# Performance work log

Measured on AMD Instinct MI355X. Metric: run time of the kernel, lower is better.

## Reference

```python
import jax, jax.numpy as jnp
import numpy as np

T, B = 4096, 32
EP_LEN = 256
K = T // EP_LEN          # episodes per trajectory
LM = EP_LEN              # max episode length
S_DIM, C_DIM, M_DIM, L_DIM = 128, 32, 32, 32
E_S, E_C, H, A = 128, 64, 256, 16


def setup_inputs() -> dict:
    key = jax.random.key(0)
    ks = jax.random.split(key, 16)
    f = lambda i, shape: jax.random.normal(ks[i], shape, jnp.float32)
    inp = {
        "state": f(0, (T, B, S_DIM)),
        "latent_mean": f(1, (T, B, L_DIM)) * 0.1,
        "latent_logvar": f(2, (T, B, L_DIM)) * 0.1,
        "latent_mean_t": f(3, (T, B, L_DIM)) * 0.1,
        "latent_logvar_t": f(4, (T, B, L_DIM)) * 0.1,
        "agent_character": f(5, (T, B, C_DIM)),
        "mental_state": f(6, (T, B, M_DIM)),
        "partner_actions": jax.random.randint(ks[7], (LM, B), 0, A, jnp.int32),
    }
    # episode boundaries: done at the last step of each EP_LEN-long episode
    t = jnp.arange(T)
    inp["dones"] = jnp.broadcast_to(((t + 1) % EP_LEN == 0).astype(jnp.float32)[:, None], (T, B))
    sc = lambda fan: 1.0 / np.sqrt(fan)
    inp["W_se"] = f(8, (S_DIM, E_S)) * sc(S_DIM); inp["b_se"] = jnp.zeros((E_S,), jnp.float32)
    inp["W_ce"] = f(9, (C_DIM, E_C)) * sc(C_DIM); inp["b_ce"] = jnp.zeros((E_C,), jnp.float32)
    inp["W_sa"] = f(10, (E_S + E_C, H)) * sc(E_S + E_C); inp["b_sa"] = jnp.zeros((H,), jnp.float32)
    inp["W_h"] = f(11, (E_C + M_DIM, H)) * sc(E_C + M_DIM); inp["b_h"] = jnp.zeros((H,), jnp.float32)
    inp["Wi"] = f(12, (H, 3 * H)) * sc(H); inp["bi"] = jnp.zeros((3 * H,), jnp.float32)
    inp["Wh"] = f(13, (H, 3 * H)) * sc(H); inp["bh"] = jnp.zeros((3 * H,), jnp.float32)
    inp["W_out"] = f(14, (H, A)) * sc(H); inp["b_out"] = jnp.zeros((A,), jnp.float32)
    return inp


def _gru(h, x, Wi, bi, Wh, bh):
    gi = x @ Wi + bi
    gh = h @ Wh + bh
    ir, iz, inn = jnp.split(gi, 3, axis=-1)
    hr, hz, hn = jnp.split(gh, 3, axis=-1)
    r = jax.nn.sigmoid(ir + hr)
    z = jax.nn.sigmoid(iz + hz)
    n = jnp.tanh(inn + r * hn)
    return (1.0 - z) * n + z * h


def _episode_layout(d):  # d: [T] float dones -> (episode_id, pos_in_episode)
    started = jnp.concatenate([jnp.zeros((1,), bool), d[:-1] > 0.5])
    ep = jnp.cumsum(started.astype(jnp.int32))
    t = jnp.arange(d.shape[0])
    start = jax.lax.cummax(jnp.where(started, t, 0))
    return ep, t - start


def _to_episodes(x, ep, pos):  # x: [T, F] -> [K, LM, F]  (transform_timestep_to_batch)
    return jnp.zeros((K, LM) + x.shape[1:], x.dtype).at[ep, pos].set(x, mode="drop")


def _shift_padding_to_front(out, mask):  # out: [K, LM, D], mask: [K, LM]
    cnt = mask.sum(-1).astype(jnp.int32)
    src = jnp.arange(LM)[None, :] - (LM - cnt)[:, None]
    idx = jnp.clip(src, 0, LM - 1)
    ok = (src >= 0).astype(out.dtype)
    shifted = jnp.take_along_axis(out, idx[:, :, None], axis=1) * ok[:, :, None]
    return shifted, jnp.take_along_axis(mask, idx, axis=1) * ok


def _forward(state, latent_mean, latent_logvar, latent_mean_t, latent_logvar_t,
             agent_character, mental_state, partner_actions, dones,
             W_se, b_se, W_ce, b_ce, W_sa, b_sa, W_h, b_h, Wi, bi, Wh, bh, W_out, b_out):
    # ---- KL between consecutive-timestep posteriors ----
    lm = jnp.concatenate((latent_mean, latent_mean_t), axis=-1)
    lv = jnp.concatenate((latent_logvar, latent_logvar_t), axis=-1)
    gauss_dim = lm.shape[-1]
    all_m = jnp.concatenate((jnp.zeros((1,) + lm.shape[1:], lm.dtype), lm), axis=0)
    all_lv = jnp.concatenate((jnp.zeros((1,) + lv.shape[1:], lv.dtype), lv), axis=0)
    mu, m = all_m[1:], all_m[:-1]
    logE, logS = all_lv[1:], all_lv[:-1]
    kl = 0.5 * (jnp.sum(logS, -1) - jnp.sum(logE, -1) - gauss_dim
                + jnp.sum(jnp.exp(logE - logS), -1)
                + jnp.sum((m - mu) * (m - mu) / jnp.exp(logS), -1))  # [T,B]
    kl_loss = kl.sum(0).sum(0).mean()

    # ---- embeddings ----
    se = jax.nn.relu(state @ W_se + b_se)                         # [T,B,E_S]
    ce = jax.nn.relu(agent_character @ W_ce + b_ce)               # [T,B,E_C]
    sa = jnp.concatenate((se, ce), -1) @ W_sa + b_sa              # [T,B,H]
    hid = jnp.concatenate((ce, mental_state), -1) @ W_h + b_h     # [T,B,H]

    # ---- split trajectories into episodes (gather/scatter) ----
    ep, pos = jax.vmap(_episode_layout, in_axes=1, out_axes=0)(dones)  # [B,T] each
    to_ep = jax.vmap(_to_episodes, in_axes=(1, 0, 0), out_axes=0)
    k_sa = to_ep(sa, ep, pos)                                     # [B,K,LM,H]
    k_hid = to_ep(hid, ep, pos)                                   # [B,K,LM,H]
    k_d = to_ep(dones[..., None], ep, pos)[..., 0]                # [B,K,LM]
    mask = jax.vmap(lambda e, p: jnp.zeros((K, LM), jnp.float32).at[e, p].set(1.0, mode="drop"))(ep, pos)

    # ---- sequential RNN scan per episode (vectorized over B*K) ----
    h0 = k_hid[:, :, 0, :]                                        # [B,K,H]
    xs = (jnp.moveaxis(k_sa, 2, 0), jnp.moveaxis(k_hid, 2, 0), jnp.moveaxis(k_d, 2, 0))

    def step(h, xt):
        sa_t, hid_t, d_t = xt
        h = jnp.where(d_t[..., None] > 0.5, hid_t, h)             # reset to per-step init on done
        h = _gru(h, sa_t, Wi, bi, Wh, bh)
        return h, h

    _, ys = jax.lax.scan(step, h0, xs)                            # [LM,B,K,H]
    ys = jnp.moveaxis(ys, 0, 2)                                   # [B,K,LM,H]

    logits = (ys @ W_out + b_out) * mask[..., None]               # [B,K,LM,A]
    shifted, _ = jax.vmap(_shift_padding_to_front)(logits, mask)
    out = jnp.moveaxis(shifted.sum(1), 0, 1)                      # [LM,B,A]

    logp = jnp.take_along_axis(jax.nn.log_softmax(out, -1), partner_actions[..., None], -1)[..., 0]
    return kl_loss, logp.sum(-1)                                  # scalar, [LM]


def reference(state, latent_mean, latent_logvar, latent_mean_t, latent_logvar_t,
              agent_character, mental_state, partner_actions, dones,
              W_se, b_se, W_ce, b_ce, W_sa, b_sa, W_h, b_h, Wi, bi, Wh, bh, W_out, b_out):
    return _forward(state, latent_mean, latent_logvar, latent_mean_t, latent_logvar_t,
                    agent_character, mental_state, partner_actions, dones,
                    W_se, b_se, W_ce, b_ce, W_sa, b_sa, W_h, b_h, Wi, bi, Wh, bh, W_out, b_out)
```

## Files before the change

### kernel.cpp

```cpp
#include <hip/hip_runtime.h>
#include <math.h>

typedef short bf16x8 __attribute__((ext_vector_type(8)));
typedef float f32x4 __attribute__((ext_vector_type(4)));
typedef unsigned short u16;
typedef unsigned int u32;

#define T_DIM 4096
#define B_DIM 32

static constexpr size_t OFF_SE     = 0;
static constexpr size_t OFF_CE     = 33554432;
static constexpr size_t OFF_SA     = 50331648;
static constexpr size_t OFF_HID    = 117440512;
static constexpr size_t OFF_WHT    = 117964800;
static constexpr size_t OFF_WIT    = 118358016;
static constexpr size_t OFF_OUTACC = 118751232;
static constexpr size_t OFF_KLP    = 119799808;

__device__ __forceinline__ u16 f2bf(float x) {
    u32 b = __float_as_uint(x);
    u32 lsb = (b >> 16) & 1u;
    b += 0x7fffu + lsb;
    return (u16)(b >> 16);
}
__device__ __forceinline__ float bf2f(u16 u) {
    return __uint_as_float(((u32)u) << 16);
}
__device__ __forceinline__ float fsig(float x) {
    x = fminf(fmaxf(x, -30.f), 30.f);
    float e = __expf(x);
    return __fdividef(e, e + 1.f);
}
__device__ __forceinline__ float ftanh(float x) {
    x = fminf(fmaxf(x, -15.f), 15.f);
    float e = __expf(2.f * x);
    return __fdividef(e - 1.f, e + 1.f);
}

__global__ __launch_bounds__(256) void prep_kernel(const float* __restrict__ Wh,
                                                   const float* __restrict__ Wi,
                                                   u16* __restrict__ WhT,
                                                   u16* __restrict__ WiT) {
    int idx = blockIdx.x * 256 + threadIdx.x;
    if (idx < 196608) {
        int n = idx >> 8, k = idx & 255;
        WhT[idx] = f2bf(Wh[k * 768 + n]);
    } else {
        int i = idx - 196608;
        int n = i >> 8, k = i & 255;
        WiT[i] = f2bf(Wi[k * 768 + n]);
    }
}

#define KLTERM(MU, LE, M, LS)                   \
    do {                                        \
        float _ls = (LS), _le = (LE);           \
        sS += _ls; sE += _le;                   \
        float _es = expf(-_ls);                 \
        sX += expf(_le) * _es;                  \
        float _dm = (M) - (MU);                 \
        sQ += _dm * _dm * _es;                  \
    } while (0)

__global__ __launch_bounds__(256) void kl_kernel(const float* __restrict__ lm,
                                                 const float* __restrict__ lv,
                                                 const float* __restrict__ lmt,
                                                 const float* __restrict__ lvt,
                                                 float* __restrict__ klp) {
    __shared__ float red[256];
    int tid = threadIdx.x;
    int idx = blockIdx.x * 256 + tid;
    float sS = 0.f, sE = 0.f, sX = 0.f, sQ = 0.f;
    const int cur = idx * 32;
    const int prv = cur - B_DIM * 32;
    const bool hasprev = (idx >= B_DIM);
    for (int half = 0; half < 2; half++) {
        const float* pm = half ? lmt : lm;
        const float* pv = half ? lvt : lv;
        for (int ch = 0; ch < 8; ch++) {
            float4 mu = *(const float4*)&pm[cur + ch * 4];
            float4 le = *(const float4*)&pv[cur + ch * 4];
            float4 m = make_float4(0.f, 0.f, 0.f, 0.f);
            float4 ls = make_float4(0.f, 0.f, 0.f, 0.f);
            if (hasprev) {
                m = *(const float4*)&pm[prv + ch * 4];
                ls = *(const float4*)&pv[prv + ch * 4];
            }
            KLTERM(mu.x, le.x, m.x, ls.x);
            KLTERM(mu.y, le.y, m.y, ls.y);
            KLTERM(mu.z, le.z, m.z, ls.z);
            KLTERM(mu.w, le.w, m.w, ls.w);
        }
    }
    float kl = 0.5f * (sS - sE - 64.0f + sX + sQ);
    red[tid] = kl;
    __syncthreads();
    for (int s = 128; s > 0; s >>= 1) {
        if (tid < s) red[tid] += red[tid + s];
        __syncthreads();
    }
    if (tid == 0) klp[blockIdx.x] = red[0];
}

__global__ __launch_bounds__(256) void gemm_k(const float* __restrict__ A32a,
                                              const u16* __restrict__ A16a,
                                              const u16* __restrict__ A16b,
                                              const float* __restrict__ W,
                                              const float* __restrict__ bias,
                                              u16* __restrict__ out,
                                              int mode, int K, int N, int do_relu) {
    __shared__ __align__(16) u16 As[64 * 40];
    __shared__ __align__(16) u16 Bs[64 * 40];
    const int tid = threadIdx.x;
    const int rows0 = blockIdx.x * 64;
    const int cols0 = blockIdx.y * 64;
    const int w16 = tid >> 6;
    const int lane = tid & 63;
    const int quad = lane >> 4;
    const int l15 = lane & 15;
    f32x4 acc[4];
    for (int i = 0; i < 4; i++) acc[i] = (f32x4){0.f, 0.f, 0.f, 0.f};
    const int nsteps = K >> 5;
    const int arow = tid >> 2, aseg = (tid & 3) << 3;
    const int bk = tid >> 3, bseg = (tid & 7) << 3;
    for (int ks = 0; ks < nsteps; ks++) {
        const int grow = rows0 + arow;
        const int k0 = ks * 32 + aseg;
        if (mode == 0) {
            float4 v0 = *(const float4*)&A32a[grow * 128 + k0];
            float4 v1 = *(const float4*)&A32a[grow * 128 + k0 + 4];
            u16* d = &As[arow * 40 + aseg];
            d[0] = f2bf(v0.x); d[1] = f2bf(v0.y); d[2] = f2bf(v0.z); d[3] = f2bf(v0.w);
            d[4] = f2bf(v1.x); d[5] = f2bf(v1.y); d[6] = f2bf(v1.z); d[7] = f2bf(v1.w);
        } else if (mode == 1) {
            float4 v0 = *(const float4*)&A32a[grow * 32 + k0];
            float4 v1 = *(const float4*)&A32a[grow * 32 + k0 + 4];
            u16* d = &As[arow * 40 + aseg];
            d[0] = f2bf(v0.x); d[1] = f2bf(v0.y); d[2] = f2bf(v0.z); d[3] = f2bf(v0.w);
            d[4] = f2bf(v1.x); d[5] = f2bf(v1.y); d[6] = f2bf(v1.z); d[7] = f2bf(v1.w);
        } else if (mode == 2) {
            bf16x8 v = (k0 < 128) ? *(const bf16x8*)&A16a[grow * 128 + k0]
                                  : *(const bf16x8*)&A16b[grow * 64 + (k0 - 128)];
            *(bf16x8*)&As[arow * 40 + aseg] = v;
        } else {
            const int k6 = grow >> 6, w = (grow >> 5) & 1, bb = grow & 31;
            const int trow = (k6 * 256 + w * 255) * B_DIM + bb;
            for (int j = 0; j < 8; j++) {
                const int k = k0 + j;
                float v = (k < 64) ? bf2f(A16a[trow * 64 + k]) : A32a[trow * 32 + (k - 64)];
                As[arow * 40 + aseg + j] = f2bf(v);
            }
        }
        const int gk = ks * 32 + bk;
        {
            float4 w0 = *(const float4*)&W[gk * N + cols0 + bseg];
            float4 w1 = *(const float4*)&W[gk * N + cols0 + bseg + 4];
            Bs[(bseg + 0) * 40 + bk] = f2bf(w0.x);
            Bs[(bseg + 1) * 40 + bk] = f2bf(w0.y);
            Bs[(bseg + 2) * 40 + bk] = f2bf(w0.z);
            Bs[(bseg + 3) * 40 + bk] = f2bf(w0.w);
            Bs[(bseg + 4) * 40 + bk] = f2bf(w1.x);
            Bs[(bseg + 5) * 40 + bk] = f2bf(w1.y);
            Bs[(bseg + 6) * 40 + bk] = f2bf(w1.z);
            Bs[(bseg + 7) * 40 + bk] = f2bf(w1.w);
        }
        __syncthreads();
        bf16x8 af = *(const bf16x8*)&As[(w16 * 16 + l15) * 40 + quad * 8];
        for (int nt = 0; nt < 4; nt++) {
            bf16x8 bfr = *(const bf16x8*)&Bs[(nt * 16 + l15) * 40 + quad * 8];
            acc[nt] = __builtin_amdgcn_mfma_f32_16x16x32_bf16(af, bfr, acc[nt], 0, 0, 0);
        }
        __syncthreads();
    }
    for (int nt = 0; nt < 4; nt++) {
        const int c = cols0 + nt * 16 + l15;
        const float bv = bias[c];
        for (int r = 0; r < 4; r++) {
            const int row = rows0 + w16 * 16 + quad * 4 + r;
            float v = acc[nt][r] + bv;
            if (do_relu) v = fmaxf(v, 0.f);
            out[row * N + c] = f2bf(v);
        }
    }
}

__global__ void __launch_bounds__(512)
__attribute__((amdgpu_waves_per_eu(2, 2)))
gru6_kernel(const u16* __restrict__ hid,
            const u16* __restrict__ sa,
            const u16* __restrict__ WhT,
            const u16* __restrict__ WiT,
            const float* __restrict__ Wout,
            const float* __restrict__ bi,
            const float* __restrict__ bh,
            u16* __restrict__ gic_all,
            float* __restrict__ outacc) {
    __shared__ __align__(16) u16 whL[8 * 16 * 264];
    __shared__ __align__(16) u16 stage[64 * 264];
    __shared__ __align__(16) u16 hB[16 * 264];
    __shared__ __align__(16) u16 WoL[16 * 264];
    __shared__ float bfold[768];
    __shared__ float bhnL[256];
    const int blk = blockIdx.x;
    const int b = blk >> 1, half = blk & 1;
    const int tid = threadIdx.x;
    const int lane = tid & 63, wv = tid >> 6;
    const int quad = lane >> 4, l15 = lane & 15;
    const int c0 = (tid & 63) * 4;
    u16* gic = gic_all + (size_t)blk * (256 * 768);

    for (int i = tid; i < 4096; i += 512) {
        const int s = i >> 9, rr = (i >> 5) & 15, seg = (i & 31) * 8;
        const int g = s * 6 + 5;
        *(bf16x8*)&whL[(s * 16 + rr) * 264 + seg] = *(const bf16x8*)&WhT[(g * 16 + rr) * 256 + seg];
    }
    for (int i = tid; i < 4096; i += 512) {
        const int a = i >> 8, k = i & 255;
        WoL[a * 264 + k] = f2bf(Wout[k * 16 + a]);
    }
    for (int c = tid; c < 768; c += 512) bfold[c] = (c < 512) ? (bi[c] + bh[c]) : bi[c];
    if (tid < 256) bhnL[tid] = bh[512 + tid];
    float hreg[4];
    {
        ushort4 hv = *(const ushort4*)&hid[(size_t)((((half << 3) + wv) << 6) + b) * 256 + c0];
        hreg[0] = bf2f(hv.x); hreg[1] = bf2f(hv.y);
        hreg[2] = bf2f(hv.z); hreg[3] = bf2f(hv.w);
        *(ushort4*)&hB[wv * 264 + c0] = hv;
        ushort4 z = make_ushort4(0, 0, 0, 0);
        *(ushort4*)&hB[(8 + wv) * 264 + c0] = z;
    }
    __syncthreads();

    bf16x8 wreg[5][8];
    for (int ch = 0; ch < 8; ch++) {
        for (int as = 0; as < 4; as++) {
            __syncthreads();
#pragma unroll
            for (int j = 0; j < 4; j++) {
                const int lin = j * 512 + tid;
                const int row = lin >> 5, seg = (lin & 31) * 8;
                const int pcs = as * 8 + (row >> 3), sql = row & 7;
                const int t = ((half << 3) + sql) * 256 + ch * 32 + pcs;
                *(bf16x8*)&stage[row * 264 + seg] =
                    *(const bf16x8*)&sa[((size_t)(t * 32 + b)) * 256 + seg];
            }
            __syncthreads();
            bf16x8 afr[4][8];
#pragma unroll
            for (int mt = 0; mt < 4; mt++)
#pragma unroll
                for (int ks = 0; ks < 8; ks++)
                    afr[mt][ks] = *(const bf16x8*)&stage[(mt * 16 + l15) * 264 + ks * 32 + quad * 8];
            bf16x8 wc[8], wn[8];
            {
                const u16* p = &WiT[((wv * 6) * 16 + l15) * 256 + quad * 8];
#pragma unroll
                for (int ks = 0; ks < 8; ks++) wc[ks] = *(const bf16x8*)&p[ks * 32];
            }
            for (int j = 0; j < 6; j++) {
                if (j < 5) {
                    const u16* p = &WiT[((wv * 6 + j + 1) * 16 + l15) * 256 + quad * 8];
#pragma unroll
                    for (int ks = 0; ks < 8; ks++) wn[ks] = *(const bf16x8*)&p[ks * 32];
                }
                const float bf = bfold[(wv * 6 + j) * 16 + l15];
#pragma unroll
                for (int mt = 0; mt < 4; mt++) {
                    f32x4 acc = (f32x4){0.f, 0.f, 0.f, 0.f};
#pragma unroll
                    for (int ks = 0; ks < 8; ks++)
                        acc = __builtin_amdgcn_mfma_f32_16x16x32_bf16(afr[mt][ks], wc[ks], acc, 0, 0, 0);
                    const int rbase = as * 64 + mt * 16 + quad * 4;
#pragma unroll
                    for (int r = 0; r < 4; r++)
                        gic[(size_t)(rbase + r) * 768 + (wv * 6 + j) * 16 + l15] = f2bf(acc[r] + bf);
                }
#pragma unroll
                for (int ks = 0; ks < 8; ks++) wc[ks] = wn[ks];
            }
        }
#pragma unroll
        for (int j = 0; j < 5; j++) {
            const u16* p = &WhT[((wv * 6 + j) * 16 + l15) * 256 + quad * 8];
#pragma unroll
            for (int ks = 0; ks < 8; ks++) wreg[j][ks] = *(const bf16x8*)&p[ks * 32];
        }
        for (int pc = 0; pc < 32; pc++) {
            const int POS = ch * 32 + pc;
            __syncthreads();
            const u16* gp = &gic[(size_t)(pc * 8 + wv) * 768];
            ushort4 g_r = *(const ushort4*)&gp[c0];
            ushort4 g_z = *(const ushort4*)&gp[256 + c0];
            ushort4 g_n = *(const ushort4*)&gp[512 + c0];
            bf16x8 af[8];
            if (POS == 255) {
                const u16* hp = &hid[(size_t)((((half << 3) + (l15 & 7)) << 6) + 32 + b) * 256 + quad * 8];
#pragma unroll
                for (int ks = 0; ks < 8; ks++) af[ks] = *(const bf16x8*)&hp[ks * 32];
            } else {
#pragma unroll
                for (int ks = 0; ks < 8; ks++)
                    af[ks] = *(const bf16x8*)&hB[l15 * 264 + ks * 32 + quad * 8];
            }
            if (wv == 7 && POS > 0) {
                f32x4 acc = (f32x4){0.f, 0.f, 0.f, 0.f};
#pragma unroll
                for (int ks = 0; ks < 8; ks++) {
                    bf16x8 al = *(const bf16x8*)&hB[l15 * 264 + ks * 32 + quad * 8];
                    bf16x8 wo = *(const bf16x8*)&WoL[l15 * 264 + ks * 32 + quad * 8];
                    acc = __builtin_amdgcn_mfma_f32_16x16x32_bf16(al, wo, acc, 0, 0, 0);
                }
                float s = acc[0] + acc[1] + acc[2] + acc[3];
                s += __shfl_down(s, 32);
                s += __shfl_down(s, 16);
                if (lane < 16)
                    outacc[(size_t)half * 131072 + ((size_t)(POS - 1) * B_DIM + b) * 16 + lane] = s;
            }
#pragma unroll
            for (int j = 0; j < 5; j++) {
                f32x4 acc = (f32x4){0.f, 0.f, 0.f, 0.f};
#pragma unroll
                for (int ks = 0; ks < 8; ks++)
                    acc = __builtin_amdgcn_mfma_f32_16x16x32_bf16(af[ks], wreg[j][ks], acc, 0, 0, 0);
                const int t = wv * 6 + j;
#pragma unroll
                for (int r = 0; r < 4; r++)
                    stage[(quad * 4 + r) * 776 + t * 16 + l15] = f2bf(acc[r]);
            }
            {
                const u16* p = &whL[(wv * 16 + l15) * 264 + quad * 8];
                f32x4 acc = (f32x4){0.f, 0.f, 0.f, 0.f};
#pragma unroll
                for (int ks = 0; ks < 8; ks++)
                    acc = __builtin_amdgcn_mfma_f32_16x16x32_bf16(af[ks], *(const bf16x8*)&p[ks * 32], acc, 0, 0, 0);
                const int t = wv * 6 + 5;
#pragma unroll
                for (int r = 0; r < 4; r++)
                    stage[(quad * 4 + r) * 776 + t * 16 + l15] = f2bf(acc[r]);
            }
            __syncthreads();
            if (POS == 255) {
                ushort4 hv = *(const ushort4*)&hid[(size_t)((((half << 3) + wv) << 6) + 32 + b) * 256 + c0];
                hreg[0] = bf2f(hv.x); hreg[1] = bf2f(hv.y);
                hreg[2] = bf2f(hv.z); hreg[3] = bf2f(hv.w);
            }
            ushort4 h_r = *(const ushort4*)&stage[wv * 776 + c0];
            ushort4 h_z = *(const ushort4*)&stage[wv * 776 + 256 + c0];
            ushort4 h_n = *(const ushort4*)&stage[wv * 776 + 512 + c0];
            const u16* grp = (const u16*)&g_r; const u16* gzp = (const u16*)&g_z;
            const u16* gnp = (const u16*)&g_n;
            const u16* hrp = (const u16*)&h_r; const u16* hzp = (const u16*)&h_z;
            const u16* hnp = (const u16*)&h_n;
            ushort4 hp4;
            u16* ho = (u16*)&hp4;
#pragma unroll
            for (int j = 0; j < 4; j++) {
                const float rv = fsig(bf2f(grp[j]) + bf2f(hrp[j]));
                const float zv = fsig(bf2f(gzp[j]) + bf2f(hzp[j]));
                const float nv = ftanh(bf2f(gnp[j]) + rv * (bf2f(hnp[j]) + bhnL[c0 + j]));
                hreg[j] = (1.f - zv) * nv + zv * hreg[j];
                ho[j] = f2bf(hreg[j]);
            }
            *(ushort4*)&hB[wv * 264 + c0] = hp4;
        }
    }
    __syncthreads();
    if (wv == 7) {
        f32x4 acc = (f32x4){0.f, 0.f, 0.f, 0.f};
#pragma unroll
        for (int ks = 0; ks < 8; ks++) {
            bf16x8 al = *(const bf16x8*)&hB[l15 * 264 + ks * 32 + quad * 8];
            bf16x8 wo = *(const bf16x8*)&WoL[l15 * 264 + ks * 32 + quad * 8];
            acc = __builtin_amdgcn_mfma_f32_16x16x32_bf16(al, wo, acc, 0, 0, 0);
        }
        float s = acc[0] + acc[1] + acc[2] + acc[3];
        s += __shfl_down(s, 32);
        s += __shfl_down(s, 16);
        if (lane < 16)
            outacc[(size_t)half * 131072 + ((size_t)255 * B_DIM + b) * 16 + lane] = s;
    }
}

__global__ __launch_bounds__(64) void final_kernel(const float* __restrict__ outacc,
                                                   const int* __restrict__ pa,
                                                   const float* __restrict__ klp,
                                                   const float* __restrict__ bout,
                                                   float* __restrict__ dout) {
    const int lane = threadIdx.x;
    if (blockIdx.x == 256) {
        float s = 0.f;
        for (int j = 0; j < 8; j++) s += klp[lane + 64 * j];
        for (int off = 32; off > 0; off >>= 1) s += __shfl_down(s, off);
        if (lane == 0) dout[0] = s;
        return;
    }
    const int pos = blockIdx.x;
    float lp = 0.f;
    if (lane < 32) {
        const float* r0 = outacc + ((size_t)pos * B_DIM + lane) * 16;
        const float* r1 = r0 + 131072;
        float v[16];
        float mx = -1e30f;
#pragma unroll
        for (int a = 0; a < 16; a++) {
            v[a] = r0[a] + r1[a] + 16.0f * bout[a];
            mx = fmaxf(mx, v[a]);
        }
        float s = 0.f;
#pragma unroll
        for (int a = 0; a < 16; a++) s += expf(v[a] - mx);
        const int ai = pa[pos * B_DIM + lane];
        lp = v[ai] - mx - logf(s);
    }
    for (int off = 16; off > 0; off >>= 1) lp += __shfl_down(lp, off);
    if (lane == 0) dout[1 + pos] = lp;
}

extern "C" void kernel_launch(void* const* d_in, const int* in_sizes, int n_in,
                              void* d_out, int out_size, void* d_ws, size_t ws_size,
                              hipStream_t stream) {
    const float* state = (const float*)d_in[0];
    const float* lm    = (const float*)d_in[1];
    const float* lv    = (const float*)d_in[2];
    const float* lmt   = (const float*)d_in[3];
    const float* lvt   = (const float*)d_in[4];
    const float* ach   = (const float*)d_in[5];
    const float* ms    = (const float*)d_in[6];
    const int*   pa    = (const int*)d_in[7];
    const float* W_se  = (const float*)d_in[9];
    const float* b_se  = (const float*)d_in[10];
    const float* W_ce  = (const float*)d_in[11];
    const float* b_ce  = (const float*)d_in[12];
    const float* W_sa  = (const float*)d_in[13];
    const float* b_sa  = (const float*)d_in[14];
    const float* W_h   = (const float*)d_in[15];
    const float* b_h   = (const float*)d_in[16];
    const float* Wi    = (const float*)d_in[17];
    const float* bi    = (const float*)d_in[18];
    const float* Wh    = (const float*)d_in[19];
    const float* bh    = (const float*)d_in[20];
    const float* Wout  = (const float*)d_in[21];
    const float* bout  = (const float*)d_in[22];

    char* ws = (char*)d_ws;
    u16* se   = (u16*)(ws + OFF_SE);
    u16* ce   = (u16*)(ws + OFF_CE);
    u16* sa   = (u16*)(ws + OFF_SA);
    u16* hid  = (u16*)(ws + OFF_HID);
    u16* WhT  = (u16*)(ws + OFF_WHT);
    u16* WiT  = (u16*)(ws + OFF_WIT);
    float* outacc = (float*)(ws + OFF_OUTACC);
    float* klp    = (float*)(ws + OFF_KLP);
    float* dout   = (float*)d_out;

    prep_kernel<<<1536, 256, 0, stream>>>(Wh, Wi, WhT, WiT);
    kl_kernel<<<512, 256, 0, stream>>>(lm, lv, lmt, lvt, klp);
    gemm_k<<<dim3(2048, 2), 256, 0, stream>>>(state, nullptr, nullptr, W_se, b_se, se, 0, 128, 128, 1);
    gemm_k<<<dim3(2048, 1), 256, 0, stream>>>(ach, nullptr, nullptr, W_ce, b_ce, ce, 1, 32, 64, 1);
    gemm_k<<<dim3(2048, 4), 256, 0, stream>>>(nullptr, se, ce, W_sa, b_sa, sa, 2, 192, 256, 0);
    gemm_k<<<dim3(16, 4), 256, 0, stream>>>(ms, ce, nullptr, W_h, b_h, hid, 5, 96, 256, 0);
    gru6_kernel<<<64, 512, 0, stream>>>(hid, sa, WhT, WiT, Wout, bi, bh, se, outacc);
    final_kernel<<<257, 64, 0, stream>>>(outacc, pa, klp, bout, dout);
}
```

Baseline: 1.669 ms.

## Keep GRU gate accumulators in registers with double-buffered hidden state

Each wave now computes the r, z and n gate tiles for its own hidden columns, so the recurrent MFMA results stay in registers instead of round-tripping through LDS. This removes one of the two barriers per timestep, and the hidden state is double-buffered in LDS. LDS tiles get an XOR swizzle to cut bank conflicts, and the gic layout is interleaved so each lane fetches its r/z/n inputs in one load. The per-step output projection moves out of the recurrence: summed hidden states go to global memory and the final kernel multiplies them by W_out. The trade-off is more global writes and a heavier final kernel, and only half the lanes do the gate math.

```diff
diff --git a/kernel.cpp b/kernel.cpp
--- a/kernel.cpp
+++ b/kernel.cpp
@@ -187,48 +187,58 @@
 
 __global__ void __launch_bounds__(512)
 __attribute__((amdgpu_waves_per_eu(2, 2)))
-gru6_kernel(const u16* __restrict__ hid,
+gru8_kernel(const u16* __restrict__ hid,
             const u16* __restrict__ sa,
             const u16* __restrict__ WhT,
             const u16* __restrict__ WiT,
-            const float* __restrict__ Wout,
             const float* __restrict__ bi,
             const float* __restrict__ bh,
             u16* __restrict__ gic_all,
-            float* __restrict__ outacc) {
+            float* __restrict__ hsum) {
     __shared__ __align__(16) u16 whL[8 * 16 * 264];
     __shared__ __align__(16) u16 stage[64 * 264];
-    __shared__ __align__(16) u16 hB[16 * 264];
-    __shared__ __align__(16) u16 WoL[16 * 264];
+    __shared__ __align__(16) u16 hB[2][16 * 264];
     __shared__ float bfold[768];
-    __shared__ float bhnL[256];
     const int blk = blockIdx.x;
     const int b = blk >> 1, half = blk & 1;
     const int tid = threadIdx.x;
     const int lane = tid & 63, wv = tid >> 6;
     const int quad = lane >> 4, l15 = lane & 15;
-    const int c0 = (tid & 63) * 4;
-    u16* gic = gic_all + (size_t)blk * (256 * 768);
+    const int c0j0 = wv * 32 + l15;
+    u16* gic = gic_all + (size_t)blk * (256 * 1024);
+    const int gts[6] = {2 * wv, 2 * wv + 1, 16 + 2 * wv, 17 + 2 * wv, 32 + 2 * wv, 33 + 2 * wv};
 
     for (int i = tid; i < 4096; i += 512) {
         const int s = i >> 9, rr = (i >> 5) & 15, seg = (i & 31) * 8;
-        const int g = s * 6 + 5;
-        *(bf16x8*)&whL[(s * 16 + rr) * 264 + seg] = *(const bf16x8*)&WhT[(g * 16 + rr) * 256 + seg];
-    }
-    for (int i = tid; i < 4096; i += 512) {
-        const int a = i >> 8, k = i & 255;
-        WoL[a * 264 + k] = f2bf(Wout[k * 16 + a]);
+        const int g = 33 + 2 * s;
+        *(bf16x8*)&whL[(s * 16 + rr) * 264 + (seg ^ ((rr & 7) << 3))] =
+            *(const bf16x8*)&WhT[(g * 16 + rr) * 256 + seg];
     }
     for (int c = tid; c < 768; c += 512) bfold[c] = (c < 512) ? (bi[c] + bh[c]) : bi[c];
-    if (tid < 256) bhnL[tid] = bh[512 + tid];
-    float hreg[4];
-    {
-        ushort4 hv = *(const ushort4*)&hid[(size_t)((((half << 3) + wv) << 6) + b) * 256 + c0];
-        hreg[0] = bf2f(hv.x); hreg[1] = bf2f(hv.y);
-        hreg[2] = bf2f(hv.z); hreg[3] = bf2f(hv.w);
-        *(ushort4*)&hB[wv * 264 + c0] = hv;
-        ushort4 z = make_ushort4(0, 0, 0, 0);
-        *(ushort4*)&hB[(8 + wv) * 264 + c0] = z;
+    const float bhn0 = bh[512 + c0j0];
+    const float bhn1 = bh[512 + c0j0 + 16];
+    float hreg[2][4] = {{0.f, 0.f, 0.f, 0.f}, {0.f, 0.f, 0.f, 0.f}};
+    if (quad < 2) {
+#pragma unroll
+        for (int j = 0; j < 2; j++)
+#pragma unroll
+            for (int r = 0; r < 4; r++) {
+                const int rw = quad * 4 + r;
+                const int c = c0j0 + 16 * j;
+                u16 hv = hid[(size_t)((((half << 3) + rw) << 6) + b) * 256 + c];
+                hreg[j][r] = bf2f(hv);
+                hB[0][rw * 264 + (c ^ ((rw & 7) << 3))] = hv;
+            }
+    } else {
+#pragma unroll
+        for (int j = 0; j < 2; j++)
+#pragma unroll
+            for (int r = 0; r < 4; r++) {
+                const int rw = quad * 4 + r;
+                const int c = c0j0 + 16 * j;
+                hB[0][rw * 264 + (c ^ ((rw & 7) << 3))] = 0;
+                hB[1][rw * 264 + (c ^ ((rw & 7) << 3))] = 0;
+            }
     }
     __syncthreads();
 
@@ -242,7 +252,7 @@
                 const int row = lin >> 5, seg = (lin & 31) * 8;
                 const int pcs = as * 8 + (row >> 3), sql = row & 7;
                 const int t = ((half << 3) + sql) * 256 + ch * 32 + pcs;
-                *(bf16x8*)&stage[row * 264 + seg] =
+                *(bf16x8*)&stage[row * 264 + (seg ^ ((row & 7) << 3))] =
                     *(const bf16x8*)&sa[((size_t)(t * 32 + b)) * 256 + seg];
             }
             __syncthreads();
@@ -251,20 +261,23 @@
             for (int mt = 0; mt < 4; mt++)
 #pragma unroll
                 for (int ks = 0; ks < 8; ks++)
-                    afr[mt][ks] = *(const bf16x8*)&stage[(mt * 16 + l15) * 264 + ks * 32 + quad * 8];
+                    afr[mt][ks] = *(const bf16x8*)&stage[(mt * 16 + l15) * 264 +
+                                                         ((ks * 32 + quad * 8) ^ ((l15 & 7) << 3))];
             bf16x8 wc[8], wn[8];
             {
-                const u16* p = &WiT[((wv * 6) * 16 + l15) * 256 + quad * 8];
+                const u16* p = &WiT[(size_t)(gts[0] * 16 + l15) * 256 + quad * 8];
 #pragma unroll
                 for (int ks = 0; ks < 8; ks++) wc[ks] = *(const bf16x8*)&p[ks * 32];
             }
-            for (int j = 0; j < 6; j++) {
-                if (j < 5) {
-                    const u16* p = &WiT[((wv * 6 + j + 1) * 16 + l15) * 256 + quad * 8];
+#pragma unroll
+            for (int jj = 0; jj < 6; jj++) {
+                if (jj < 5) {
+                    const u16* p = &WiT[(size_t)(gts[jj + 1] * 16 + l15) * 256 + quad * 8];
 #pragma unroll
                     for (int ks = 0; ks < 8; ks++) wn[ks] = *(const bf16x8*)&p[ks * 32];
                 }
-                const float bf = bfold[(wv * 6 + j) * 16 + l15];
+                const float bf = bfold[gts[jj] * 16 + l15];
+                const int cp = ((2 * wv + (jj & 1)) * 16 + l15) * 4 + (jj >> 1);
 #pragma unroll
                 for (int mt = 0; mt < 4; mt++) {
                     f32x4 acc = (f32x4){0.f, 0.f, 0.f, 0.f};
@@ -274,7 +287,7 @@
                     const int rbase = as * 64 + mt * 16 + quad * 4;
 #pragma unroll
                     for (int r = 0; r < 4; r++)
-                        gic[(size_t)(rbase + r) * 768 + (wv * 6 + j) * 16 + l15] = f2bf(acc[r] + bf);
+                        gic[(size_t)(rbase + r) * 1024 + cp] = f2bf(acc[r] + bf);
                 }
 #pragma unroll
                 for (int ks = 0; ks < 8; ks++) wc[ks] = wn[ks];
@@ -282,17 +295,26 @@
         }
 #pragma unroll
         for (int j = 0; j < 5; j++) {
-            const u16* p = &WhT[((wv * 6 + j) * 16 + l15) * 256 + quad * 8];
+            const u16* p = &WhT[(size_t)(gts[j] * 16 + l15) * 256 + quad * 8];
 #pragma unroll
             for (int ks = 0; ks < 8; ks++) wreg[j][ks] = *(const bf16x8*)&p[ks * 32];
         }
+        __syncthreads();
         for (int pc = 0; pc < 32; pc++) {
             const int POS = ch * 32 + pc;
-            __syncthreads();
-            const u16* gp = &gic[(size_t)(pc * 8 + wv) * 768];
-            ushort4 g_r = *(const ushort4*)&gp[c0];
-            ushort4 g_z = *(const ushort4*)&gp[256 + c0];
-            ushort4 g_n = *(const ushort4*)&gp[512 + c0];
+            const u16* hr = hB[POS & 1];
+            u16* hw = hB[(POS + 1) & 1];
+            ushort4 gi4[2][4];
+            if (quad < 2) {
+#pragma unroll
+                for (int j = 0; j < 2; j++)
+#pragma unroll
+                    for (int r = 0; r < 4; r++) {
+                        const int rw = quad * 4 + r;
+                        gi4[j][r] = *(const ushort4*)&gic[(size_t)(pc * 8 + rw) * 1024 +
+                                                          (size_t)(c0j0 + 16 * j) * 4];
+                    }
+            }
             bf16x8 af[8];
             if (POS == 255) {
                 const u16* hp = &hid[(size_t)((((half << 3) + (l15 & 7)) << 6) + 32 + b) * 256 + quad * 8];
@@ -301,90 +323,67 @@
             } else {
 #pragma unroll
                 for (int ks = 0; ks < 8; ks++)
-                    af[ks] = *(const bf16x8*)&hB[l15 * 264 + ks * 32 + quad * 8];
-            }
-            if (wv == 7 && POS > 0) {
-                f32x4 acc = (f32x4){0.f, 0.f, 0.f, 0.f};
+                    af[ks] = *(const bf16x8*)&hr[l15 * 264 + ((ks * 32 + quad * 8) ^ ((l15 & 7) << 3))];
+            }
+            f32x4 acc[6];
+#pragma unroll
+            for (int jj = 0; jj < 6; jj++) acc[jj] = (f32x4){0.f, 0.f, 0.f, 0.f};
+#pragma unroll
+            for (int jj = 0; jj < 5; jj++)
+#pragma unroll
+                for (int ks = 0; ks < 8; ks++)
+                    acc[jj] = __builtin_amdgcn_mfma_f32_16x16x32_bf16(af[ks], wreg[jj][ks], acc[jj], 0, 0, 0);
+            {
+                const u16* p = &whL[(wv * 16 + l15) * 264];
 #pragma unroll
                 for (int ks = 0; ks < 8; ks++) {
-                    bf16x8 al = *(const bf16x8*)&hB[l15 * 264 + ks * 32 + quad * 8];
-                    bf16x8 wo = *(const bf16x8*)&WoL[l15 * 264 + ks * 32 + quad * 8];
-                    acc = __builtin_amdgcn_mfma_f32_16x16x32_bf16(al, wo, acc, 0, 0, 0);
+                    bf16x8 wf = *(const bf16x8*)&p[(ks * 32 + quad * 8) ^ ((l15 & 7) << 3)];
+                    acc[5] = __builtin_amdgcn_mfma_f32_16x16x32_bf16(af[ks], wf, acc[5], 0, 0, 0);
                 }
-                float s = acc[0] + acc[1] + acc[2] + acc[3];
-                s += __shfl_down(s, 32);
-                s += __shfl_down(s, 16);
-                if (lane < 16)
-                    outacc[(size_t)half * 131072 + ((size_t)(POS - 1) * B_DIM + b) * 16 + lane] = s;
-            }
-#pragma unroll
-            for (int j = 0; j < 5; j++) {
-                f32x4 acc = (f32x4){0.f, 0.f, 0.f, 0.f};
-#pragma unroll
-                for (int ks = 0; ks < 8; ks++)
-                    acc = __builtin_amdgcn_mfma_f32_16x16x32_bf16(af[ks], wreg[j][ks], acc, 0, 0, 0);
-                const int t = wv * 6 + j;
-#pragma unroll
-                for (int r = 0; r < 4; r++)
-                    stage[(quad * 4 + r) * 776 + t * 16 + l15] = f2bf(acc[r]);
-            }
-            {
-                const u16* p = &whL[(wv * 16 + l15) * 264 + quad * 8];
-                f32x4 acc = (f32x4){0.f, 0.f, 0.f, 0.f};
-#pragma unroll
-                for (int ks = 0; ks < 8; ks++)
-                    acc = __builtin_amdgcn_mfma_f32_16x16x32_bf16(af[ks], *(const bf16x8*)&p[ks * 32], acc, 0, 0, 0);
-                const int t = wv * 6 + 5;
-#pragma unroll
-                for (int r = 0; r < 4; r++)
-                    stage[(quad * 4 + r) * 776 + t * 16 + l15] = f2bf(acc[r]);
+            }
+            if (POS == 255 && quad < 2) {
+#pragma unroll
+                for (int j = 0; j < 2; j++)
+#pragma unroll
+                    for (int r = 0; r < 4; r++) {
+                        const int rw = quad * 4 + r;
+                        hreg[j][r] = bf2f(hid[(size_t)((((half << 3) + rw) << 6) + 32 + b) * 256 +
+                                              (c0j0 + 16 * j)]);
+                    }
+            }
+            float l4[2] = {0.f, 0.f};
+            if (quad < 2) {
+#pragma unroll
+                for (int j = 0; j < 2; j++) {
+                    const float bhn = j ? bhn1 : bhn0;
+#pragma unroll
+                    for (int r = 0; r < 4; r++) {
+                        const int rw = quad * 4 + r;
+                        const float rv = fsig(bf2f(gi4[j][r].x) + acc[j][r]);
+                        const float zv = fsig(bf2f(gi4[j][r].y) + acc[2 + j][r]);
+                        const float nv = ftanh(bf2f(gi4[j][r].z) + rv * (acc[4 + j][r] + bhn));
+                        hreg[j][r] = (1.f - zv) * nv + zv * hreg[j][r];
+                        l4[j] += hreg[j][r];
+                        hw[rw * 264 + ((c0j0 + 16 * j) ^ ((rw & 7) << 3))] = f2bf(hreg[j][r]);
+                    }
+                }
+            }
+            float t0 = l4[0] + __shfl_down(l4[0], 16);
+            float t1 = l4[1] + __shfl_down(l4[1], 16);
+            if (quad == 0) {
+                float* hp = hsum + (size_t)half * 2097152 + ((size_t)POS * 32 + b) * 256 + c0j0;
+                hp[0] = t0;
+                hp[16] = t1;
             }
             __syncthreads();
-            if (POS == 255) {
-                ushort4 hv = *(const ushort4*)&hid[(size_t)((((half << 3) + wv) << 6) + 32 + b) * 256 + c0];
-                hreg[0] = bf2f(hv.x); hreg[1] = bf2f(hv.y);
-                hreg[2] = bf2f(hv.z); hreg[3] = bf2f(hv.w);
-            }
-            ushort4 h_r = *(const ushort4*)&stage[wv * 776 + c0];
-            ushort4 h_z = *(const ushort4*)&stage[wv * 776 + 256 + c0];
-            ushort4 h_n = *(const ushort4*)&stage[wv * 776 + 512 + c0];
-            const u16* grp = (const u16*)&g_r; const u16* gzp = (const u16*)&g_z;
-            const u16* gnp = (const u16*)&g_n;
-            const u16* hrp = (const u16*)&h_r; const u16* hzp = (const u16*)&h_z;
-            const u16* hnp = (const u16*)&h_n;
-            ushort4 hp4;
-            u16* ho = (u16*)&hp4;
-#pragma unroll
-            for (int j = 0; j < 4; j++) {
-                const float rv = fsig(bf2f(grp[j]) + bf2f(hrp[j]));
-                const float zv = fsig(bf2f(gzp[j]) + bf2f(hzp[j]));
-                const float nv = ftanh(bf2f(gnp[j]) + rv * (bf2f(hnp[j]) + bhnL[c0 + j]));
-                hreg[j] = (1.f - zv) * nv + zv * hreg[j];
-                ho[j] = f2bf(hreg[j]);
-            }
-            *(ushort4*)&hB[wv * 264 + c0] = hp4;
-        }
-    }
-    __syncthreads();
-    if (wv == 7) {
-        f32x4 acc = (f32x4){0.f, 0.f, 0.f, 0.f};
-#pragma unroll
-        for (int ks = 0; ks < 8; ks++) {
-            bf16x8 al = *(const bf16x8*)&hB[l15 * 264 + ks * 32 + quad * 8];
-            bf16x8 wo = *(const bf16x8*)&WoL[l15 * 264 + ks * 32 + quad * 8];
-            acc = __builtin_amdgcn_mfma_f32_16x16x32_bf16(al, wo, acc, 0, 0, 0);
-        }
-        float s = acc[0] + acc[1] + acc[2] + acc[3];
-        s += __shfl_down(s, 32);
-        s += __shfl_down(s, 16);
-        if (lane < 16)
-            outacc[(size_t)half * 131072 + ((size_t)255 * B_DIM + b) * 16 + lane] = s;
-    }
-}
-
-__global__ __launch_bounds__(64) void final_kernel(const float* __restrict__ outacc,
+        }
+    }
+}
+
+__global__ __launch_bounds__(64) void final_kernel(const float* __restrict__ hsum,
                                                    const int* __restrict__ pa,
                                                    const float* __restrict__ klp,
+                                                   const float* __restrict__ Wout,
                                                    const float* __restrict__ bout,
                                                    float* __restrict__ dout) {
     const int lane = threadIdx.x;
@@ -395,18 +394,33 @@
         if (lane == 0) dout[0] = s;
         return;
     }
+    __shared__ float WoS[4096];
+    for (int i = lane; i < 4096; i += 64) WoS[i] = Wout[i];
+    __syncthreads();
     const int pos = blockIdx.x;
     float lp = 0.f;
     if (lane < 32) {
-        const float* r0 = outacc + ((size_t)pos * B_DIM + lane) * 16;
-        const float* r1 = r0 + 131072;
+        const float* h0 = hsum + ((size_t)pos * B_DIM + lane) * 256;
+        const float* h1 = h0 + 2097152;
         float v[16];
+#pragma unroll
+        for (int a = 0; a < 16; a++) v[a] = 16.0f * bout[a];
+        for (int k4 = 0; k4 < 64; k4++) {
+            float4 a0 = *(const float4*)&h0[k4 * 4];
+            float4 a1 = *(const float4*)&h1[k4 * 4];
+            const float hk0 = a0.x + a1.x, hk1 = a0.y + a1.y;
+            const float hk2 = a0.z + a1.z, hk3 = a0.w + a1.w;
+            const float* w0 = &WoS[(k4 * 4 + 0) * 16];
+            const float* w1 = &WoS[(k4 * 4 + 1) * 16];
+            const float* w2 = &WoS[(k4 * 4 + 2) * 16];
+            const float* w3 = &WoS[(k4 * 4 + 3) * 16];
+#pragma unroll
+            for (int a = 0; a < 16; a++)
+                v[a] += hk0 * w0[a] + hk1 * w1[a] + hk2 * w2[a] + hk3 * w3[a];
+        }
         float mx = -1e30f;
 #pragma unroll
-        for (int a = 0; a < 16; a++) {
-            v[a] = r0[a] + r1[a] + 16.0f * bout[a];
-            mx = fmaxf(mx, v[a]);
-        }
+        for (int a = 0; a < 16; a++) mx = fmaxf(mx, v[a]);
         float s = 0.f;
 #pragma unroll
         for (int a = 0; a < 16; a++) s += expf(v[a] - mx);
@@ -450,7 +464,7 @@
     u16* hid  = (u16*)(ws + OFF_HID);
     u16* WhT  = (u16*)(ws + OFF_WHT);
     u16* WiT  = (u16*)(ws + OFF_WIT);
-    float* outacc = (float*)(ws + OFF_OUTACC);
+    float* hsum   = (float*)(ws + OFF_CE);
     float* klp    = (float*)(ws + OFF_KLP);
     float* dout   = (float*)d_out;
 
@@ -460,6 +474,6 @@
     gemm_k<<<dim3(2048, 1), 256, 0, stream>>>(ach, nullptr, nullptr, W_ce, b_ce, ce, 1, 32, 64, 1);
     gemm_k<<<dim3(2048, 4), 256, 0, stream>>>(nullptr, se, ce, W_sa, b_sa, sa, 2, 192, 256, 0);
     gemm_k<<<dim3(16, 4), 256, 0, stream>>>(ms, ce, nullptr, W_h, b_h, hid, 5, 96, 256, 0);
-    gru6_kernel<<<64, 512, 0, stream>>>(hid, sa, WhT, WiT, Wout, bi, bh, se, outacc);
-    final_kernel<<<257, 64, 0, stream>>>(outacc, pa, klp, bout, dout);
-}
+    gru8_kernel<<<64, 512, 0, stream>>>(hid, sa, WhT, WiT, bi, bh, se, hsum);
+    final_kernel<<<257, 64, 0, stream>>>(hsum, pa, klp, Wout, bout, dout);
+}
```

Result: slower. 4.811 ms (+188.3%).
